# Optimization experiments

Measured on AMD Instinct MI355X. Metric: run time of the kernel, lower is better.

## Reference

```python
import jax, jax.numpy as jnp
import numpy as np
from jax import lax

DIM = 8            # per-head dim
GROUPS = 192       # 3 * heads, groups of the pointwise aggreg conv
EPS_ATT = 1e-15
EPS_BN = 1e-5


def conv1x1(x, w):
    # x: (B,C,H,W), w: (O,C)
    return jnp.einsum('bchw,oc->bohw', x, w)


def setup_inputs() -> dict:
    key = jax.random.key(0)
    ks = jax.random.split(key, 9)
    B, C, H, W = 4, 512, 64, 64
    td3 = 3 * 512  # 3 * total_dim = 1536
    return {
        'x':       jax.random.normal(ks[0], (B, C, H, W), jnp.float32),
        'w_qkv':   jax.random.normal(ks[1], (td3, C), jnp.float32) * 0.05,
        'w_dw':    jax.random.normal(ks[2], (td3, 1, 5, 5), jnp.float32) * 0.05,
        'w_pw':    jax.random.normal(ks[3], (GROUPS, 8, 8), jnp.float32) * 0.05,
        'w_proj':  jax.random.normal(ks[4], (512, 1024), jnp.float32) * 0.05,
        'bn_gamma': 1.0 + 0.1 * jax.random.normal(ks[5], (512,), jnp.float32),
        'bn_beta': 0.1 * jax.random.normal(ks[6], (512,), jnp.float32),
        'bn_mean': 0.1 * jax.random.normal(ks[7], (512,), jnp.float32),
        'bn_var':  0.5 + jax.random.uniform(ks[8], (512,), jnp.float32),
    }


def reference(x, w_qkv, w_dw, w_pw, w_proj, bn_gamma, bn_beta, bn_mean, bn_var):
    B, _, H, W = x.shape
    # qkv 1x1 conv (no norm / act)
    qkv = conv1x1(x, w_qkv)                      # (B,1536,H,W)
    # multi-scale aggreg branch: depthwise 5x5 then grouped 1x1
    y = lax.conv_general_dilated(
        qkv, w_dw, window_strides=(1, 1), padding=((2, 2), (2, 2)),
        feature_group_count=qkv.shape[1],
        dimension_numbers=('NCHW', 'OIHW', 'NCHW'))
    yg = y.reshape(B, GROUPS, 8, H, W)
    y = jnp.einsum('bgihw,goi->bgohw', yg, w_pw).reshape(B, -1, H, W)
    ms = jnp.concatenate([qkv, y], axis=1)       # (B,3072,H,W)

    # relu linear attention (fp32)
    N = H * W
    t = ms.astype(jnp.float32).reshape(B, -1, 3 * DIM, N)   # (B,128,24,N)
    q = jax.nn.relu(t[:, :, :DIM])               # (B,h,8,N)
    k = jax.nn.relu(t[:, :, DIM:2 * DIM])        # (B,h,8,N)
    v = t[:, :, 2 * DIM:]                        # (B,h,8,N)
    v = jnp.concatenate([v, jnp.ones_like(v[:, :, :1])], axis=2)  # (B,h,9,N)
    vk = jnp.einsum('bhdn,bhen->bhde', v, k)     # (B,h,9,8)
    out = jnp.einsum('bhde,bhen->bhdn', vk, q)   # (B,h,9,N)
    out = out[:, :, :DIM] / (out[:, :, DIM:] + EPS_ATT)
    out = out.reshape(B, -1, H, W).astype(ms.dtype)  # (B,1024,H,W)

    # proj 1x1 conv + BatchNorm2d (inference, running stats)
    p = conv1x1(out, w_proj)                     # (B,512,H,W)
    scale = (bn_gamma / jnp.sqrt(bn_var + EPS_BN))[None, :, None, None]
    shift = (bn_beta - bn_mean * bn_gamma / jnp.sqrt(bn_var + EPS_BN))[None, :, None, None]
    return p * scale + shift
```

## Files before the change

kernel.cpp:

```cpp
#include <hip/hip_runtime.h>
#include <cstddef>


#define NPIX 4096
#define TD3 1536

typedef _Float16 f16;
typedef __attribute__((ext_vector_type(8))) _Float16 v8h;
typedef __attribute__((ext_vector_type(4))) float v4f;
typedef unsigned short ushort_t;

#define GLL16(g, l) __builtin_amdgcn_global_load_lds(                         \
    (const __attribute__((address_space(1))) unsigned int*)(g),               \
    (__attribute__((address_space(3))) unsigned int*)(l), 16, 0, 0)

template <int SPLITB, int BN>
__global__ __launch_bounds__(256) void gemm_f16(
    const f16* __restrict__ Ah, const f16* __restrict__ Al,
    const f16* __restrict__ Bh, const f16* __restrict__ Bl,
    float* __restrict__ C, int M, int N, int K,
    const float* __restrict__ bn_g, const float* __restrict__ bn_b,
    const float* __restrict__ bn_m, const float* __restrict__ bn_v)
{
    __shared__ f16 AsH[2][128 * 32];
    __shared__ f16 AsL[2][128 * 32];
    __shared__ f16 BsH[2][128 * 32];
    __shared__ f16 BsL[SPLITB ? 2 : 1][SPLITB ? 128 * 32 : 64];

    const int tid  = threadIdx.x;
    const int lane = tid & 63;
    const int w    = tid >> 6;
    const int wm   = w >> 1, wn = w & 1;
    const int mBase = blockIdx.y * 128, nBase = blockIdx.x * 128;
    Bh += (size_t)blockIdx.z * N * K;
    if (SPLITB) Bl += (size_t)blockIdx.z * N * K;
    C  += (size_t)blockIdx.z * M * N;

    const f16* gAh[2]; const f16* gAl[2]; const f16* gBh[2]; const f16* gBl[2];
    int ldsOff[2];
    #pragma unroll
    for (int p = 0; p < 2; ++p) {
        int phys = (w * 2 + p) * 1024 + lane * 16;
        int lgc  = phys ^ (((phys >> 7) & 3) << 4);
        int r  = lgc >> 6;
        int ci = (lgc & 63) >> 1;
        gAh[p] = Ah + (size_t)(mBase + r) * K + ci;
        gAl[p] = Al + (size_t)(mBase + r) * K + ci;
        gBh[p] = Bh + (size_t)(nBase + r) * K + ci;
        if (SPLITB) gBl[p] = Bl + (size_t)(nBase + r) * K + ci;
        ldsOff[p] = (w * 2 + p) * 512;
    }

    const int kq = lane >> 4;
    const int rm = lane & 15;
    const int slot = kq ^ ((rm >> 1) & 3);

    v4f acc[4][4];
    #pragma unroll
    for (int i = 0; i < 4; ++i)
        #pragma unroll
        for (int j = 0; j < 4; ++j)
            acc[i][j] = (v4f){0.f, 0.f, 0.f, 0.f};

    const int KT = K >> 5;

    #pragma unroll
    for (int p = 0; p < 2; ++p) {
        GLL16(gAh[p], &AsH[0][ldsOff[p]]);
        GLL16(gAl[p], &AsL[0][ldsOff[p]]);
        GLL16(gBh[p], &BsH[0][ldsOff[p]]);
        if (SPLITB) GLL16(gBl[p], &BsL[0][ldsOff[p]]);
    }
    __syncthreads();

    for (int kt = 0; kt < KT; ++kt) {
        const int cb = kt & 1, nb = cb ^ 1;
        if (kt + 1 < KT) {
            #pragma unroll
            for (int p = 0; p < 2; ++p) {
                GLL16(gAh[p] + (kt + 1) * 32, &AsH[nb][ldsOff[p]]);
                GLL16(gAl[p] + (kt + 1) * 32, &AsL[nb][ldsOff[p]]);
                GLL16(gBh[p] + (kt + 1) * 32, &BsH[nb][ldsOff[p]]);
                if (SPLITB) GLL16(gBl[p] + (kt + 1) * 32, &BsL[nb][ldsOff[p]]);
            }
        }

        v8h ah[4], al[4], bh[4], bl[4];
        #pragma unroll
        for (int i = 0; i < 4; ++i) {
            int rowA = wm * 64 + i * 16 + rm;
            int rowB = wn * 64 + i * 16 + rm;
            ah[i] = *(const v8h*)&AsH[cb][rowA * 32 + slot * 8];
            al[i] = *(const v8h*)&AsL[cb][rowA * 32 + slot * 8];
            bh[i] = *(const v8h*)&BsH[cb][rowB * 32 + slot * 8];
            if (SPLITB)
                bl[i] = *(const v8h*)&BsL[cb][rowB * 32 + slot * 8];
        }
        #pragma unroll
        for (int i = 0; i < 4; ++i)
            #pragma unroll
            for (int j = 0; j < 4; ++j) {
                acc[i][j] = __builtin_amdgcn_mfma_f32_16x16x32_f16(
                    ah[i], bh[j], acc[i][j], 0, 0, 0);
                acc[i][j] = __builtin_amdgcn_mfma_f32_16x16x32_f16(
                    al[i], bh[j], acc[i][j], 0, 0, 0);
                if (SPLITB)
                    acc[i][j] = __builtin_amdgcn_mfma_f32_16x16x32_f16(
                        ah[i], bl[j], acc[i][j], 0, 0, 0);
            }
        __syncthreads();
    }

    const int rq = lane >> 4, cn = lane & 15;
    #pragma unroll
    for (int i = 0; i < 4; ++i) {
        #pragma unroll
        for (int rg = 0; rg < 4; ++rg) {
            int row = mBase + wm * 64 + i * 16 + rq * 4 + rg;
            float sc = 1.f, sh = 0.f;
            if (BN) {
                sc = bn_g[row] * rsqrtf(bn_v[row] + 1e-5f);
                sh = bn_b[row] - bn_m[row] * sc;
            }
            #pragma unroll
            for (int j = 0; j < 4; ++j) {
                int col = nBase + wn * 64 + j * 16 + cn;
                float v = acc[i][j][rg];
                C[(size_t)row * N + col] = BN ? (v * sc + sh) : v;
            }
        }
    }
}

__global__ __launch_bounds__(256) void cvt_split(
    const float* __restrict__ src, f16* __restrict__ dh, f16* __restrict__ dl,
    int n4)
{
    int i = blockIdx.x * 256 + threadIdx.x;
    if (i < n4) {
        float4 f = ((const float4*)src)[i];
        f16 h[4], l[4];
        float ff[4] = {f.x, f.y, f.z, f.w};
        #pragma unroll
        for (int q = 0; q < 4; ++q) {
            h[q] = (f16)ff[q];
            l[q] = (f16)(ff[q] - (float)h[q]);
        }
        *(uint2*)&dh[(size_t)i * 4] = *(uint2*)h;
        *(uint2*)&dl[(size_t)i * 4] = *(uint2*)l;
    }
}

__global__ __launch_bounds__(256) void transp_split(
    const float* __restrict__ src, f16* __restrict__ dh, f16* __restrict__ dl)
{
    __shared__ float t[64][65];
    const int tid = threadIdx.x;
    const int n0 = blockIdx.x * 64, c0 = blockIdx.y * 64, b = blockIdx.z;

    const int row = tid >> 2;
    const int nn  = (tid & 3) * 16;
    const float* sp = src + ((size_t)b * 512 + c0 + row) * NPIX + n0 + nn;
    #pragma unroll
    for (int q = 0; q < 4; ++q) {
        float4 f = *(const float4*)(sp + q * 4);
        t[row][nn + q * 4 + 0] = f.x;
        t[row][nn + q * 4 + 1] = f.y;
        t[row][nn + q * 4 + 2] = f.z;
        t[row][nn + q * 4 + 3] = f.w;
    }
    __syncthreads();

    const int nrow = tid >> 2;
    const int cc   = (tid & 3) * 16;
    f16 h[16], l[16];
    #pragma unroll
    for (int q = 0; q < 16; ++q) {
        float f = t[cc + q][nrow];
        h[q] = (f16)f;
        l[q] = (f16)(f - (float)h[q]);
    }
    size_t di = ((size_t)b * NPIX + n0 + nrow) * 512 + c0 + cc;
    *(uint4*)&dh[di] = *(uint4*)&h[0];
    *(uint4*)&dh[di + 8] = *(uint4*)&h[8];
    *(uint4*)&dl[di] = *(uint4*)&l[0];
    *(uint4*)&dl[di + 8] = *(uint4*)&l[8];
}

__global__ __launch_bounds__(256) void dwpw(
    const float* __restrict__ qkv, const float* __restrict__ w_dw,
    const float* __restrict__ w_pw, float* __restrict__ y)
{
    __shared__ float tile[8][36][68];

    const int tid = threadIdx.x;
    const int g = blockIdx.y;
    const int b = blockIdx.z;
    const int h0 = blockIdx.x * 32;
    const size_t cbase = (size_t)b * TD3 + g * 8;

    for (int idx = tid; idx < 288; idx += 256) {
        int ch = idx / 36, r = idx - ch * 36;
        *(float2*)&tile[ch][r][0]  = (float2){0.f, 0.f};
        *(float2*)&tile[ch][r][66] = (float2){0.f, 0.f};
    }
    #pragma unroll
    for (int it = 0; it < 18; ++it) {
        int idx = tid + it * 256;
        int ch = idx / 576;
        int rem = idx - ch * 576;
        int r = rem >> 4, q = rem & 15;
        int gh = h0 + r - 2;
        float4 v = {0.f, 0.f, 0.f, 0.f};
        if (gh >= 0 && gh < 64)
            v = *(const float4*)&qkv[(cbase + ch) * NPIX + gh * 64 + q * 4];
        *(float2*)&tile[ch][r][2 + q * 4] = (float2){v.x, v.y};
        *(float2*)&tile[ch][r][4 + q * 4] = (float2){v.z, v.w};
    }
    __syncthreads();

    const int wc0 = (tid & 15) * 4;
    const int rp  = tid >> 4;

    float acc[8][8];
    #pragma unroll
    for (int o = 0; o < 8; ++o)
        #pragma unroll
        for (int p = 0; p < 8; ++p) acc[o][p] = 0.f;

    #pragma unroll
    for (int ch = 0; ch < 8; ++ch) {
        const float* wdg = w_dw + (size_t)(g * 8 + ch) * 25;
        float wdr[25];
        #pragma unroll
        for (int t = 0; t < 25; ++t) wdr[t] = wdg[t];
        float wpr[8];
        #pragma unroll
        for (int o = 0; o < 8; ++o) wpr[o] = w_pw[g * 64 + o * 8 + ch];

        float w[6][8];
        #pragma unroll
        for (int rr = 0; rr < 6; ++rr) {
            *(float4*)&w[rr][0] = *(const float4*)&tile[ch][rp * 2 + rr][wc0];
            *(float4*)&w[rr][4] = *(const float4*)&tile[ch][rp * 2 + rr][wc0 + 4];
        }

        float dwv[8];
        #pragma unroll
        for (int s = 0; s < 2; ++s)
            #pragma unroll
            for (int cc = 0; cc < 4; ++cc) {
                float sum = 0.f;
                #pragma unroll
                for (int di = 0; di < 5; ++di)
                    #pragma unroll
                    for (int dj = 0; dj < 5; ++dj)
                        sum = fmaf(w[s + di][cc + dj], wdr[di * 5 + dj], sum);
                dwv[s * 4 + cc] = sum;
            }
        #pragma unroll
        for (int o = 0; o < 8; ++o)
            #pragma unroll
            for (int p = 0; p < 8; ++p)
                acc[o][p] = fmaf(dwv[p], wpr[o], acc[o][p]);
    }

    #pragma unroll
    for (int o = 0; o < 8; ++o)
        #pragma unroll
        for (int s = 0; s < 2; ++s) {
            float4 v = {acc[o][s * 4 + 0], acc[o][s * 4 + 1],
                        acc[o][s * 4 + 2], acc[o][s * 4 + 3]};
            *(float4*)&y[(cbase + o) * NPIX + (h0 + rp * 2 + s) * 64 + wc0] = v;
        }
}

__global__ __launch_bounds__(256) void attn_stats(
    const float* __restrict__ qkv, const float* __restrict__ yy,
    float* __restrict__ vkout)
{
    const int h = blockIdx.x;
    const int b = blockIdx.y;
    const float* src = (h < 64)
        ? qkv + ((size_t)b * TD3 + h * 24) * NPIX
        : yy  + ((size_t)b * TD3 + (h - 64) * 24) * NPIX;

    float acc[9][8];
    #pragma unroll
    for (int d = 0; d < 9; ++d)
        #pragma unroll
        for (int e = 0; e < 8; ++e) acc[d][e] = 0.f;

    for (int n = threadIdx.x; n < NPIX; n += 256) {
        float kr[8], vv[8];
        #pragma unroll
        for (int e = 0; e < 8; ++e) kr[e] = fmaxf(src[(8 + e) * NPIX + n], 0.f);
        #pragma unroll
        for (int d = 0; d < 8; ++d) vv[d] = src[(16 + d) * NPIX + n];
        #pragma unroll
        for (int d = 0; d < 8; ++d)
            #pragma unroll
            for (int e = 0; e < 8; ++e) acc[d][e] = fmaf(vv[d], kr[e], acc[d][e]);
        #pragma unroll
        for (int e = 0; e < 8; ++e) acc[8][e] += kr[e];
    }

    __shared__ float part[4][72];
    const int lane = threadIdx.x & 63, wave = threadIdx.x >> 6;
    #pragma unroll
    for (int i = 0; i < 72; ++i) {
        float v = acc[i / 8][i % 8];
        #pragma unroll
        for (int off = 32; off; off >>= 1) v += __shfl_down(v, off, 64);
        if (lane == 0) part[wave][i] = v;
    }
    __syncthreads();
    if (threadIdx.x < 72) {
        float v = part[0][threadIdx.x] + part[1][threadIdx.x] +
                  part[2][threadIdx.x] + part[3][threadIdx.x];
        vkout[((size_t)b * 128 + h) * 72 + threadIdx.x] = v;
    }
}

__global__ __launch_bounds__(256) void attn_apply_t(
    const float* __restrict__ qkv, const float* __restrict__ yy,
    const float* __restrict__ vkin, f16* __restrict__ attout)
{
    const int h = blockIdx.y;
    const int b = blockIdx.z;
    const int n = blockIdx.x * 256 + threadIdx.x;

    __shared__ float vk[72];
    if (threadIdx.x < 72)
        vk[threadIdx.x] = vkin[((size_t)b * 128 + h) * 72 + threadIdx.x];
    __syncthreads();

    const float* src = (h < 64)
        ? qkv + ((size_t)b * TD3 + h * 24) * NPIX
        : yy  + ((size_t)b * TD3 + (h - 64) * 24) * NPIX;

    float qr[8];
    #pragma unroll
    for (int e = 0; e < 8; ++e) qr[e] = fmaxf(src[e * NPIX + n], 0.f);

    float den = 0.f;
    #pragma unroll
    for (int e = 0; e < 8; ++e) den = fmaf(vk[64 + e], qr[e], den);
    float inv = 1.f / (den + 1e-15f);

    f16 o[8];
    #pragma unroll
    for (int d = 0; d < 8; ++d) {
        float num = 0.f;
        #pragma unroll
        for (int e = 0; e < 8; ++e) num = fmaf(vk[d * 8 + e], qr[e], num);
        o[d] = (f16)(num * inv);
    }
    *(uint4*)&attout[((size_t)b * NPIX + n) * 1024 + h * 8] = *(uint4*)o;
}

extern "C" void kernel_launch(void* const* d_in, const int* in_sizes, int n_in,
                              void* d_out, int out_size, void* d_ws, size_t ws_size,
                              hipStream_t stream)
{
    (void)in_sizes; (void)n_in; (void)out_size; (void)ws_size;
    const float* x      = (const float*)d_in[0];
    const float* w_qkv  = (const float*)d_in[1];
    const float* w_dw   = (const float*)d_in[2];
    const float* w_pw   = (const float*)d_in[3];
    const float* w_proj = (const float*)d_in[4];
    const float* bn_g   = (const float*)d_in[5];
    const float* bn_b   = (const float*)d_in[6];
    const float* bn_m   = (const float*)d_in[7];
    const float* bn_v   = (const float*)d_in[8];
    float* out = (float*)d_out;

    char* ws = (char*)d_ws;
    float* qkv     = (float*)(ws);
    float* y       = (float*)(ws + 100663296);
    f16*   x_t_h   = (f16*)(ws + 201326592);
    f16*   x_t_l   = (f16*)(ws + 218103808);
    f16*   attout  = (f16*)(ws + 201326592);
    f16*   w_qkv_h = (f16*)(ws + 234881024);
    f16*   w_qkv_l = (f16*)(ws + 236453888);
    f16*   w_proj_h= (f16*)(ws + 238026752);
    f16*   w_proj_l= (f16*)(ws + 239075328);
    float* vk      = out;

    cvt_split<<<768, 256, 0, stream>>>(w_qkv, w_qkv_h, w_qkv_l, 196608);
    cvt_split<<<512, 256, 0, stream>>>(w_proj, w_proj_h, w_proj_l, 131072);
    transp_split<<<dim3(64, 8, 4), 256, 0, stream>>>(x, x_t_h, x_t_l);
    gemm_f16<1, 0><<<dim3(32, 12, 4), 256, 0, stream>>>(
        w_qkv_h, w_qkv_l, x_t_h, x_t_l, qkv, 1536, 4096, 512,
        nullptr, nullptr, nullptr, nullptr);
    dwpw<<<dim3(2, 192, 4), 256, 0, stream>>>(qkv, w_dw, w_pw, y);
    attn_stats<<<dim3(128, 4), 256, 0, stream>>>(qkv, y, vk);
    attn_apply_t<<<dim3(16, 128, 4), 256, 0, stream>>>(qkv, y, vk, attout);
    gemm_f16<0, 1><<<dim3(32, 4, 4), 256, 0, stream>>>(
        w_proj_h, w_proj_l, attout, nullptr, out, 512, 4096, 1024,
        bn_g, bn_b, bn_m, bn_v);
}
```

Measured before the change: 341.4 us.

## Enlarge GEMM tiles to 256x128 with 512 threads and triple-buffered LDS pipeline

Measured after the change: 349.8 us. 2.5% more time.

```diff
diff --git a/kernel.cpp b/kernel.cpp
--- a/kernel.cpp
+++ b/kernel.cpp
@@ -14,42 +14,44 @@
     (const __attribute__((address_space(1))) unsigned int*)(g),               \
     (__attribute__((address_space(3))) unsigned int*)(l), 16, 0, 0)
 
+#define WAIT_VM(n) asm volatile("s_waitcnt vmcnt(" #n ")" ::: "memory")
+
 template <int SPLITB, int BN>
-__global__ __launch_bounds__(256) void gemm_f16(
+__global__ __launch_bounds__(512, 1) void gemm_f16(
     const f16* __restrict__ Ah, const f16* __restrict__ Al,
     const f16* __restrict__ Bh, const f16* __restrict__ Bl,
     float* __restrict__ C, int M, int N, int K,
     const float* __restrict__ bn_g, const float* __restrict__ bn_b,
     const float* __restrict__ bn_m, const float* __restrict__ bn_v)
 {
-    __shared__ f16 AsH[2][128 * 32];
-    __shared__ f16 AsL[2][128 * 32];
-    __shared__ f16 BsH[2][128 * 32];
-    __shared__ f16 BsL[SPLITB ? 2 : 1][SPLITB ? 128 * 32 : 64];
+    __shared__ f16 AsH[3][256 * 32];
+    __shared__ f16 AsL[3][256 * 32];
+    __shared__ f16 BsH[3][128 * 32];
+    __shared__ f16 BsL[SPLITB ? 3 : 1][SPLITB ? 128 * 32 : 32];
 
     const int tid  = threadIdx.x;
     const int lane = tid & 63;
     const int w    = tid >> 6;
     const int wm   = w >> 1, wn = w & 1;
-    const int mBase = blockIdx.y * 128, nBase = blockIdx.x * 128;
+    const int mBase = blockIdx.y * 256, nBase = blockIdx.x * 128;
     Bh += (size_t)blockIdx.z * N * K;
     if (SPLITB) Bl += (size_t)blockIdx.z * N * K;
     C  += (size_t)blockIdx.z * M * N;
 
-    const f16* gAh[2]; const f16* gAl[2]; const f16* gBh[2]; const f16* gBl[2];
-    int ldsOff[2];
+    int aOff[2], ldsA[2];
     #pragma unroll
     for (int p = 0; p < 2; ++p) {
         int phys = (w * 2 + p) * 1024 + lane * 16;
         int lgc  = phys ^ (((phys >> 7) & 3) << 4);
         int r  = lgc >> 6;
         int ci = (lgc & 63) >> 1;
-        gAh[p] = Ah + (size_t)(mBase + r) * K + ci;
-        gAl[p] = Al + (size_t)(mBase + r) * K + ci;
-        gBh[p] = Bh + (size_t)(nBase + r) * K + ci;
-        if (SPLITB) gBl[p] = Bl + (size_t)(nBase + r) * K + ci;
-        ldsOff[p] = (w * 2 + p) * 512;
-    }
+        aOff[p] = (mBase + r) * K + ci;
+        ldsA[p] = (w * 2 + p) * 512;
+    }
+    int physB = w * 1024 + lane * 16;
+    int lgcB  = physB ^ (((physB >> 7) & 3) << 4);
+    const int bOff = (nBase + (lgcB >> 6)) * K + ((lgcB & 63) >> 1);
+    const int ldsB = w * 512;
 
     const int kq = lane >> 4;
     const int rm = lane & 15;
@@ -64,37 +66,41 @@
 
     const int KT = K >> 5;
 
-    #pragma unroll
-    for (int p = 0; p < 2; ++p) {
-        GLL16(gAh[p], &AsH[0][ldsOff[p]]);
-        GLL16(gAl[p], &AsL[0][ldsOff[p]]);
-        GLL16(gBh[p], &BsH[0][ldsOff[p]]);
-        if (SPLITB) GLL16(gBl[p], &BsL[0][ldsOff[p]]);
-    }
-    __syncthreads();
+    auto stage = [&](int kt, int s) {
+        const int ko = kt * 32;
+        GLL16(Ah + aOff[0] + ko, &AsH[s][ldsA[0]]);
+        GLL16(Ah + aOff[1] + ko, &AsH[s][ldsA[1]]);
+        GLL16(Al + aOff[0] + ko, &AsL[s][ldsA[0]]);
+        GLL16(Al + aOff[1] + ko, &AsL[s][ldsA[1]]);
+        GLL16(Bh + bOff + ko, &BsH[s][ldsB]);
+        if (SPLITB) GLL16(Bl + bOff + ko, &BsL[s][ldsB]);
+    };
+
+    stage(0, 0);
+    stage(1, 1);
 
     for (int kt = 0; kt < KT; ++kt) {
-        const int cb = kt & 1, nb = cb ^ 1;
-        if (kt + 1 < KT) {
-            #pragma unroll
-            for (int p = 0; p < 2; ++p) {
-                GLL16(gAh[p] + (kt + 1) * 32, &AsH[nb][ldsOff[p]]);
-                GLL16(gAl[p] + (kt + 1) * 32, &AsL[nb][ldsOff[p]]);
-                GLL16(gBh[p] + (kt + 1) * 32, &BsH[nb][ldsOff[p]]);
-                if (SPLITB) GLL16(gBl[p] + (kt + 1) * 32, &BsL[nb][ldsOff[p]]);
-            }
+        const int cs = kt % 3;
+        if (kt < KT - 1) {
+            if (SPLITB) WAIT_VM(6); else WAIT_VM(5);
+        } else {
+            WAIT_VM(0);
         }
+        __builtin_amdgcn_s_barrier();
+        __builtin_amdgcn_sched_barrier(0);
+
+        if (kt + 2 < KT) stage(kt + 2, (kt + 2) % 3);
 
         v8h ah[4], al[4], bh[4], bl[4];
         #pragma unroll
         for (int i = 0; i < 4; ++i) {
             int rowA = wm * 64 + i * 16 + rm;
             int rowB = wn * 64 + i * 16 + rm;
-            ah[i] = *(const v8h*)&AsH[cb][rowA * 32 + slot * 8];
-            al[i] = *(const v8h*)&AsL[cb][rowA * 32 + slot * 8];
-            bh[i] = *(const v8h*)&BsH[cb][rowB * 32 + slot * 8];
+            ah[i] = *(const v8h*)&AsH[cs][rowA * 32 + slot * 8];
+            al[i] = *(const v8h*)&AsL[cs][rowA * 32 + slot * 8];
+            bh[i] = *(const v8h*)&BsH[cs][rowB * 32 + slot * 8];
             if (SPLITB)
-                bl[i] = *(const v8h*)&BsL[cb][rowB * 32 + slot * 8];
+                bl[i] = *(const v8h*)&BsL[cs][rowB * 32 + slot * 8];
         }
         #pragma unroll
         for (int i = 0; i < 4; ++i)
@@ -108,7 +114,7 @@
                     acc[i][j] = __builtin_amdgcn_mfma_f32_16x16x32_f16(
                         ah[i], bl[j], acc[i][j], 0, 0, 0);
             }
-        __syncthreads();
+        __builtin_amdgcn_sched_barrier(0);
     }
 
     const int rq = lane >> 4, cn = lane & 15;
@@ -132,23 +138,27 @@
     }
 }
 
-__global__ __launch_bounds__(256) void cvt_split(
-    const float* __restrict__ src, f16* __restrict__ dh, f16* __restrict__ dl,
-    int n4)
+__global__ __launch_bounds__(256) void cvt_split2(
+    const float* __restrict__ s1, f16* __restrict__ d1h, f16* __restrict__ d1l,
+    int n4_1,
+    const float* __restrict__ s2, f16* __restrict__ d2h, f16* __restrict__ d2l,
+    int n4_2)
 {
     int i = blockIdx.x * 256 + threadIdx.x;
-    if (i < n4) {
-        float4 f = ((const float4*)src)[i];
-        f16 h[4], l[4];
-        float ff[4] = {f.x, f.y, f.z, f.w};
-        #pragma unroll
-        for (int q = 0; q < 4; ++q) {
-            h[q] = (f16)ff[q];
-            l[q] = (f16)(ff[q] - (float)h[q]);
-        }
-        *(uint2*)&dh[(size_t)i * 4] = *(uint2*)h;
-        *(uint2*)&dl[(size_t)i * 4] = *(uint2*)l;
-    }
+    const float* src; f16* dh; f16* dl; int idx;
+    if (i < n4_1) { src = s1; dh = d1h; dl = d1l; idx = i; }
+    else if (i < n4_1 + n4_2) { src = s2; dh = d2h; dl = d2l; idx = i - n4_1; }
+    else return;
+    float4 f = ((const float4*)src)[idx];
+    f16 h[4], l[4];
+    float ff[4] = {f.x, f.y, f.z, f.w};
+    #pragma unroll
+    for (int q = 0; q < 4; ++q) {
+        h[q] = (f16)ff[q];
+        l[q] = (f16)(ff[q] - (float)h[q]);
+    }
+    *(uint2*)&dh[(size_t)idx * 4] = *(uint2*)h;
+    *(uint2*)&dl[(size_t)idx * 4] = *(uint2*)l;
 }
 
 __global__ __launch_bounds__(256) void transp_split(
@@ -387,16 +397,17 @@
     f16*   w_proj_l= (f16*)(ws + 239075328);
     float* vk      = out;
 
-    cvt_split<<<768, 256, 0, stream>>>(w_qkv, w_qkv_h, w_qkv_l, 196608);
-    cvt_split<<<512, 256, 0, stream>>>(w_proj, w_proj_h, w_proj_l, 131072);
+    cvt_split2<<<1280, 256, 0, stream>>>(
+        w_qkv, w_qkv_h, w_qkv_l, 196608,
+        w_proj, w_proj_h, w_proj_l, 131072);
     transp_split<<<dim3(64, 8, 4), 256, 0, stream>>>(x, x_t_h, x_t_l);
-    gemm_f16<1, 0><<<dim3(32, 12, 4), 256, 0, stream>>>(
+    gemm_f16<1, 0><<<dim3(32, 6, 4), 512, 0, stream>>>(
         w_qkv_h, w_qkv_l, x_t_h, x_t_l, qkv, 1536, 4096, 512,
         nullptr, nullptr, nullptr, nullptr);
     dwpw<<<dim3(2, 192, 4), 256, 0, stream>>>(qkv, w_dw, w_pw, y);
     attn_stats<<<dim3(128, 4), 256, 0, stream>>>(qkv, y, vk);
     attn_apply_t<<<dim3(16, 128, 4), 256, 0, stream>>>(qkv, y, vk, attout);
-    gemm_f16<0, 1><<<dim3(32, 4, 4), 256, 0, stream>>>(
+    gemm_f16<0, 1><<<dim3(32, 2, 4), 512, 0, stream>>>(
         w_proj_h, w_proj_l, attout, nullptr, out, 512, 4096, 1024,
         bn_g, bn_b, bn_m, bn_v);
 }
```
